# Performance work log

Hardware: AMD Instinct MI355X
Metric: run time of the kernel (lower is better)

## Reference

```python
import jax, jax.numpy as jnp
import numpy as np

TAU = 1.0
EPS = 1e-10  # gumbel numerical floor


def rotation_6d_to_matrix(d6):
    # d6: [..., 6] -> [..., 3, 3] (rows b1,b2,b3), Gram-Schmidt (pytorch3d convention)
    a1, a2 = d6[..., :3], d6[..., 3:]
    b1 = a1 / jnp.linalg.norm(a1, axis=-1, keepdims=True)
    a2p = a2 - jnp.sum(b1 * a2, axis=-1, keepdims=True) * b1
    b2 = a2p / jnp.linalg.norm(a2p, axis=-1, keepdims=True)
    b3 = jnp.cross(b1, b2)
    return jnp.stack([b1, b2, b3], axis=-2)


def setup_inputs() -> dict:
    key = jax.random.key(0)
    ks = jax.random.split(key, 8)
    N, P, T = 65536, 16, 32
    cano_pc = jax.random.normal(ks[0], (N, 3), jnp.float32)
    w1 = jax.random.normal(ks[1], (128, 3), jnp.float32) * 0.3
    b1 = jnp.zeros((128,), jnp.float32)
    w2 = jax.random.normal(ks[2], (P, 128), jnp.float32) * 0.1
    b2 = jnp.zeros((P,), jnp.float32)
    proposal_6d = jnp.tile(jnp.array([1., 0., 0., 0., 1., 0.], jnp.float32), (T, P, 1)) \
        + 0.1 * jax.random.normal(ks[3], (T, P, 6), jnp.float32)
    proposal_t = 0.1 * jax.random.normal(ks[4], (T, P, 3), jnp.float32)
    # precomputed standard Gumbel noise for determinism
    u = jax.random.uniform(ks[5], (N, P), jnp.float32, minval=EPS, maxval=1.0 - EPS)
    gumbel = -jnp.log(-jnp.log(u))
    return {"cano_pc": cano_pc, "w1": w1, "b1": b1, "w2": w2, "b2": b2,
            "proposal_6d": proposal_6d, "proposal_t": proposal_t, "gumbel": gumbel}


def reference(cano_pc, w1, b1, w2, b2, proposal_6d, proposal_t, gumbel):
    T, P, _ = proposal_6d.shape
    N = cano_pc.shape[0]
    # seg_head: 1x1 Conv1d MLP 3 -> 128 -> P over N points
    h = jax.nn.relu(cano_pc @ w1.T + b1)           # [N,128]
    seg = h @ w2.T + b2                            # [N,P]
    # hard gumbel-softmax (straight-through); fwd value is exact one-hot
    y = jax.nn.softmax((seg + gumbel) / TAU, axis=-1)
    hard = jax.nn.one_hot(jnp.argmax(y, axis=-1), P, dtype=y.dtype)
    weight = hard + y - jax.lax.stop_gradient(y)   # [N,P]
    # per-(frame,part) rigid transforms
    R = rotation_6d_to_matrix(proposal_6d.reshape(-1, 6)).reshape(T, P, 3, 3)
    t = proposal_t                                 # [T,P,3]
    # dense apply: cano @ R^T + t for all (T,P)  -> [T,P,N,3]
    pc_trans = jnp.einsum('ni,tpji->tpnj', cano_pc, R) + t[:, :, None, :]
    # weighted combine over parts (weight is one-hot per point) -> [T,N,3]
    pc_out = jnp.einsum('np,tpnj->tnj', weight, pc_trans)
    # 4x4 transforms
    top = jnp.concatenate([R, t[..., None]], axis=-1)        # [T,P,3,4]
    bottom = jnp.broadcast_to(jnp.array([0., 0., 0., 1.], top.dtype), (T, P, 1, 4))
    trans_list = jnp.concatenate([top, bottom], axis=-2)     # [T,P,4,4]
    return pc_out, jnp.argmax(seg, axis=-1), trans_list
```

## Files before the change

### kernel.cpp

```cpp
#include <hip/hip_runtime.h>

#define N_PTS 65536
#define T_DIM 32
#define P_DIM 16

__global__ void prep_kernel(const float* __restrict__ d6,
                            const float* __restrict__ pt,
                            const float* __restrict__ w1,
                            const float* __restrict__ b1,
                            const float* __restrict__ w2,
                            const float* __restrict__ b2,
                            float* __restrict__ ws,
                            float* __restrict__ out_trans)
{
    int idx = blockIdx.x * blockDim.x + threadIdx.x;
    if (idx < T_DIM * P_DIM) {
        const float* a = d6 + idx * 6;
        float a1x=a[0], a1y=a[1], a1z=a[2], a2x=a[3], a2y=a[4], a2z=a[5];
        float n1 = sqrtf(a1x*a1x + a1y*a1y + a1z*a1z);
        float b1x=a1x/n1, b1y=a1y/n1, b1z=a1z/n1;
        float d = b1x*a2x + b1y*a2y + b1z*a2z;
        float px = a2x - d*b1x, py = a2y - d*b1y, pz = a2z - d*b1z;
        float n2 = sqrtf(px*px + py*py + pz*pz);
        float b2x=px/n2, b2y=py/n2, b2z=pz/n2;
        float b3x = b1y*b2z - b1z*b2y;
        float b3y = b1z*b2x - b1x*b2z;
        float b3z = b1x*b2y - b1y*b2x;
        float t0 = pt[idx*3+0], t1 = pt[idx*3+1], t2 = pt[idx*3+2];
        float* R = ws + idx*12;
        R[0]=b1x; R[1]=b1y; R[2]=b1z;
        R[3]=b2x; R[4]=b2y; R[5]=b2z;
        R[6]=b3x; R[7]=b3y; R[8]=b3z;
        R[9]=t0;  R[10]=t1; R[11]=t2;
        float* o = out_trans + idx*16;
        o[0]=b1x; o[1]=b1y; o[2]=b1z;  o[3]=t0;
        o[4]=b2x; o[5]=b2y; o[6]=b2z;  o[7]=t1;
        o[8]=b3x; o[9]=b3y; o[10]=b3z; o[11]=t2;
        o[12]=0.f; o[13]=0.f; o[14]=0.f; o[15]=1.f;
    }
    int k = idx - 512;
    if (k >= 0 && k < 128) {
        float* wp = ws + 6144 + k*20;
        wp[0]=w1[k*3+0]; wp[1]=w1[k*3+1]; wp[2]=w1[k*3+2]; wp[3]=b1[k];
        #pragma unroll
        for (int p=0;p<16;p++) wp[4+p] = w2[p*128+k];
    }
    if (idx < 16) ws[6144+2560+idx] = b2[idx];
}

__global__ __launch_bounds__(256) void main_kernel(
    const float* __restrict__ pc,
    const float* __restrict__ gumbel,
    const float* __restrict__ ws,
    float* __restrict__ out_pc,
    float* __restrict__ out_idx)
{
    __shared__ __align__(16) float s_Rt[6144];
    int tid = threadIdx.x;
    {
        const float4* src = (const float4*)ws;
        float4* dst = (float4*)s_Rt;
        for (int i = tid; i < 1536; i += 256) dst[i] = src[i];
    }
    __syncthreads();

    int n = blockIdx.x * 256 + tid;
    float x0 = pc[n*3+0], x1 = pc[n*3+1], x2 = pc[n*3+2];

    const float* wpack = ws + 6144;
    float seg[16];
    #pragma unroll
    for (int p=0;p<16;p++) seg[p] = wpack[2560+p];

    #pragma unroll 4
    for (int k=0;k<128;k++) {
        const float* wp = wpack + k*20;
        float h = fmaf(wp[0], x0, wp[3]);
        h = fmaf(wp[1], x1, h);
        h = fmaf(wp[2], x2, h);
        h = fmaxf(h, 0.0f);
        #pragma unroll
        for (int p=0;p<16;p++) seg[p] = fmaf(wp[4+p], h, seg[p]);
    }

    float best = seg[0]; int pseg = 0;
    #pragma unroll
    for (int p=1;p<16;p++) { if (seg[p] > best) { best = seg[p]; pseg = p; } }
    out_idx[n] = (float)pseg;

    float g[16];
    {
        const float4* g4 = (const float4*)(gumbel + n*16);
        #pragma unroll
        for (int j=0;j<4;j++) { float4 v = g4[j]; g[4*j]=v.x; g[4*j+1]=v.y; g[4*j+2]=v.z; g[4*j+3]=v.w; }
    }
    float bestg = seg[0] + g[0]; int pstar = 0;
    #pragma unroll
    for (int p=1;p<16;p++) { float v = seg[p] + g[p]; if (v > bestg) { bestg = v; pstar = p; } }

    const float* Rb = s_Rt + pstar*12;
    for (int t=0;t<T_DIM;t++) {
        const float* R = Rb + t*192;
        float4 r0 = *(const float4*)(R);
        float4 r1 = *(const float4*)(R+4);
        float4 r2 = *(const float4*)(R+8);
        float y0 = fmaf(r0.x, x0, r2.y); y0 = fmaf(r0.y, x1, y0); y0 = fmaf(r0.z, x2, y0);
        float y1 = fmaf(r0.w, x0, r2.z); y1 = fmaf(r1.x, x1, y1); y1 = fmaf(r1.y, x2, y1);
        float y2 = fmaf(r1.z, x0, r2.w); y2 = fmaf(r1.w, x1, y2); y2 = fmaf(r2.x, x2, y2);
        float* o = out_pc + (t * N_PTS + n) * 3;
        o[0]=y0; o[1]=y1; o[2]=y2;
    }
}

extern "C" void kernel_launch(void* const* d_in, const int* in_sizes, int n_in,
                              void* d_out, int out_size, void* d_ws, size_t ws_size,
                              hipStream_t stream)
{
    const float* pc  = (const float*)d_in[0];
    const float* w1  = (const float*)d_in[1];
    const float* b1  = (const float*)d_in[2];
    const float* w2  = (const float*)d_in[3];
    const float* b2  = (const float*)d_in[4];
    const float* d6  = (const float*)d_in[5];
    const float* pt  = (const float*)d_in[6];
    const float* gum = (const float*)d_in[7];
    float* out = (float*)d_out;
    float* ws  = (float*)d_ws;

    float* out_pc    = out;
    float* out_idx   = out + 6291456;
    float* out_trans = out + 6291456 + 65536;

    prep_kernel<<<3, 256, 0, stream>>>(d6, pt, w1, b1, w2, b2, ws, out_trans);
    main_kernel<<<256, 256, 0, stream>>>(pc, gum, ws, out_pc, out_idx);
}
```

Before: 98.15 us.

## Split MLP hidden dim and frame loop across four wavefronts per block

Each block now handles 64 points, with each of its four wavefronts computing a quarter of the 128 hidden units. Partial logits are reduced through shared memory, and wavefront 0 does the argmax and Gumbel selection. The 32 output frames are then split 8 per wavefront. The rigid-transform table is padded to a 14-float stride to cut LDS bank conflicts. This quadruples the grid to 1024 blocks for more parallelism and less per-thread serial work, at the cost of extra barriers and a shared-memory reduction.

```diff
diff --git a/kernel.cpp b/kernel.cpp
--- a/kernel.cpp
+++ b/kernel.cpp
@@ -27,11 +27,12 @@
         float b3y = b1z*b2x - b1x*b2z;
         float b3z = b1x*b2y - b1y*b2x;
         float t0 = pt[idx*3+0], t1 = pt[idx*3+1], t2 = pt[idx*3+2];
-        float* R = ws + idx*12;
+        float* R = ws + idx*14;
         R[0]=b1x; R[1]=b1y; R[2]=b1z;
         R[3]=b2x; R[4]=b2y; R[5]=b2z;
         R[6]=b3x; R[7]=b3y; R[8]=b3z;
         R[9]=t0;  R[10]=t1; R[11]=t2;
+        R[12]=0.f; R[13]=0.f;
         float* o = out_trans + idx*16;
         o[0]=b1x; o[1]=b1y; o[2]=b1z;  o[3]=t0;
         o[4]=b2x; o[5]=b2y; o[6]=b2z;  o[7]=t1;
@@ -40,41 +41,42 @@
     }
     int k = idx - 512;
     if (k >= 0 && k < 128) {
-        float* wp = ws + 6144 + k*20;
+        float* wp = ws + 7168 + k*20;
         wp[0]=w1[k*3+0]; wp[1]=w1[k*3+1]; wp[2]=w1[k*3+2]; wp[3]=b1[k];
         #pragma unroll
         for (int p=0;p<16;p++) wp[4+p] = w2[p*128+k];
     }
-    if (idx < 16) ws[6144+2560+idx] = b2[idx];
+    if (idx < 16) ws[9728+idx] = b2[idx];
 }
 
-__global__ __launch_bounds__(256) void main_kernel(
+__global__ __launch_bounds__(256) void fused_kernel(
     const float* __restrict__ pc,
     const float* __restrict__ gumbel,
     const float* __restrict__ ws,
     float* __restrict__ out_pc,
     float* __restrict__ out_idx)
 {
-    __shared__ __align__(16) float s_Rt[6144];
-    int tid = threadIdx.x;
-    {
-        const float4* src = (const float4*)ws;
-        float4* dst = (float4*)s_Rt;
-        for (int i = tid; i < 1536; i += 256) dst[i] = src[i];
+    __shared__ __align__(16) float smem[7168 + 64];
+    const int tid  = threadIdx.x;
+    const int lane = tid & 63;
+    const int wv   = __builtin_amdgcn_readfirstlane(tid >> 6);
+    const int n    = blockIdx.x * 64 + lane;
+
+    const float x0 = pc[n*3+0], x1 = pc[n*3+1], x2 = pc[n*3+2];
+
+    const float* wpk = ws + 7168 + wv*32*20;
+    float seg[16];
+    if (wv == 0) {
+        const float* b2p = ws + 9728;
+        #pragma unroll
+        for (int p=0;p<16;p++) seg[p] = b2p[p];
+    } else {
+        #pragma unroll
+        for (int p=0;p<16;p++) seg[p] = 0.f;
     }
-    __syncthreads();
-
-    int n = blockIdx.x * 256 + tid;
-    float x0 = pc[n*3+0], x1 = pc[n*3+1], x2 = pc[n*3+2];
-
-    const float* wpack = ws + 6144;
-    float seg[16];
-    #pragma unroll
-    for (int p=0;p<16;p++) seg[p] = wpack[2560+p];
-
-    #pragma unroll 4
-    for (int k=0;k<128;k++) {
-        const float* wp = wpack + k*20;
+    #pragma unroll 8
+    for (int k=0;k<32;k++) {
+        const float* wp = wpk + k*20;
         float h = fmaf(wp[0], x0, wp[3]);
         h = fmaf(wp[1], x1, h);
         h = fmaf(wp[2], x2, h);
@@ -82,32 +84,58 @@
         #pragma unroll
         for (int p=0;p<16;p++) seg[p] = fmaf(wp[4+p], h, seg[p]);
     }
+    #pragma unroll
+    for (int p=0;p<16;p++) smem[wv*1024 + p*64 + lane] = seg[p];
+    __syncthreads();
 
-    float best = seg[0]; int pseg = 0;
-    #pragma unroll
-    for (int p=1;p<16;p++) { if (seg[p] > best) { best = seg[p]; pseg = p; } }
-    out_idx[n] = (float)pseg;
+    if (wv == 0) {
+        float s[16];
+        #pragma unroll
+        for (int p=0;p<16;p++) {
+            float v = smem[p*64 + lane] + smem[1024 + p*64 + lane];
+            v += smem[2048 + p*64 + lane] + smem[3072 + p*64 + lane];
+            s[p] = v;
+        }
+        float best = s[0]; int pseg = 0;
+        #pragma unroll
+        for (int p=1;p<16;p++) { if (s[p] > best) { best = s[p]; pseg = p; } }
+        out_idx[n] = (float)pseg;
 
-    float g[16];
-    {
-        const float4* g4 = (const float4*)(gumbel + n*16);
+        float g[16];
+        const float4* g4 = (const float4*)(gumbel + (size_t)n*16);
         #pragma unroll
         for (int j=0;j<4;j++) { float4 v = g4[j]; g[4*j]=v.x; g[4*j+1]=v.y; g[4*j+2]=v.z; g[4*j+3]=v.w; }
+        float bg = s[0] + g[0]; int pstar = 0;
+        #pragma unroll
+        for (int p=1;p<16;p++) { float v = s[p] + g[p]; if (v > bg) { bg = v; pstar = p; } }
+        smem[7168 + lane] = (float)pstar;
     }
-    float bestg = seg[0] + g[0]; int pstar = 0;
+    __syncthreads();
+
+    {
+        const float2* src = (const float2*)ws;
+        float2* dst = (float2*)smem;
+        #pragma unroll
+        for (int i=0;i<14;i++) dst[tid + i*256] = src[tid + i*256];
+    }
+    __syncthreads();
+
+    const int p = (int)smem[7168 + lane];
+    const float* Rb = smem + p*14;
     #pragma unroll
-    for (int p=1;p<16;p++) { float v = seg[p] + g[p]; if (v > bestg) { bestg = v; pstar = p; } }
-
-    const float* Rb = s_Rt + pstar*12;
-    for (int t=0;t<T_DIM;t++) {
-        const float* R = Rb + t*192;
-        float4 r0 = *(const float4*)(R);
-        float4 r1 = *(const float4*)(R+4);
-        float4 r2 = *(const float4*)(R+8);
-        float y0 = fmaf(r0.x, x0, r2.y); y0 = fmaf(r0.y, x1, y0); y0 = fmaf(r0.z, x2, y0);
-        float y1 = fmaf(r0.w, x0, r2.z); y1 = fmaf(r1.x, x1, y1); y1 = fmaf(r1.y, x2, y1);
-        float y2 = fmaf(r1.z, x0, r2.w); y2 = fmaf(r1.w, x1, y2); y2 = fmaf(r2.x, x2, y2);
-        float* o = out_pc + (t * N_PTS + n) * 3;
+    for (int i=0;i<8;i++) {
+        const int t = wv*8 + i;
+        const float* R = Rb + t*224;
+        float2 r01 = *(const float2*)(R);
+        float2 r23 = *(const float2*)(R+2);
+        float2 r45 = *(const float2*)(R+4);
+        float2 r67 = *(const float2*)(R+6);
+        float2 r8t = *(const float2*)(R+8);
+        float2 t12 = *(const float2*)(R+10);
+        float y0 = fmaf(r01.x, x0, r8t.y); y0 = fmaf(r01.y, x1, y0); y0 = fmaf(r23.x, x2, y0);
+        float y1 = fmaf(r23.y, x0, t12.x); y1 = fmaf(r45.x, x1, y1); y1 = fmaf(r45.y, x2, y1);
+        float y2 = fmaf(r67.x, x0, t12.y); y2 = fmaf(r67.y, x1, y2); y2 = fmaf(r8t.x, x2, y2);
+        float* o = out_pc + ((size_t)t * N_PTS + n) * 3;
         o[0]=y0; o[1]=y1; o[2]=y2;
     }
 }
@@ -132,5 +160,5 @@
     float* out_trans = out + 6291456 + 65536;
 
     prep_kernel<<<3, 256, 0, stream>>>(d6, pt, w1, b1, w2, b2, ws, out_trans);
-    main_kernel<<<256, 256, 0, stream>>>(pc, gum, ws, out_pc, out_idx);
+    fused_kernel<<<1024, 256, 0, stream>>>(pc, gum, ws, out_pc, out_idx);
 }
```

New measurement: 87.66 us. -10.7%, faster.
